# Kernel tuning notes

Measured on AMD Instinct MI355X. Metric: run time of the kernel, lower is better.

## Reference

```python
import jax, jax.numpy as jnp
import numpy as np
import math

D_MODEL = 64
N_HEADS = 4
D_HEAD = D_MODEL // N_HEADS
SCALE = math.sqrt(D_HEAD)
B, NQ, NK = 32, 16384, 31


def setup_inputs() -> dict:
    key = jax.random.key(0)
    kq, kk, kv, km, kw, kb = jax.random.split(key, 6)
    Q = jax.random.normal(kq, (B, NQ, D_MODEL), dtype=jnp.float32)
    K = jax.random.normal(kk, (B, NK, D_MODEL), dtype=jnp.float32)
    V = jax.random.normal(kv, (B, NK, D_MODEL), dtype=jnp.float32)
    mask = jax.random.randint(km, (B, NK), 0, 2).astype(jnp.bool_)
    # out_proj: nn.Linear(d_model, d_model)
    lim = 1.0 / math.sqrt(D_MODEL)
    W_out = jax.random.uniform(kw, (D_MODEL, D_MODEL), minval=-lim, maxval=lim, dtype=jnp.float32)
    b_out = jax.random.uniform(kb, (D_MODEL,), minval=-lim, maxval=lim, dtype=jnp.float32)
    return {"Q": Q, "K": K, "V": V, "mask": mask, "W_out": W_out, "b_out": b_out}


def reference(Q, K, V, mask, W_out, b_out):
    Bn, Nq, D = Q.shape
    Nk = K.shape[1]
    # (B, H, N, d_head)
    q = Q.reshape(Bn, Nq, N_HEADS, D_HEAD).transpose(0, 2, 1, 3)
    k = K.reshape(Bn, Nk, N_HEADS, D_HEAD).transpose(0, 2, 1, 3)
    v = V.reshape(Bn, Nk, N_HEADS, D_HEAD).transpose(0, 2, 1, 3)
    # (B, H, Nq, Nk)
    attn = jnp.einsum('bhqd,bhkd->bhqk', q, k) / SCALE
    attn = jnp.where(mask[:, None, None, :], attn, -jnp.inf)
    attn = jax.nn.softmax(attn, axis=-1)
    attn = jnp.nan_to_num(attn, nan=0.0)
    out = jnp.einsum('bhqk,bhkd->bhqd', attn, v)
    out = out.transpose(0, 2, 1, 3).reshape(Bn, Nq, D)
    return out @ W_out.T + b_out
```

## Files before the change

kernel.cpp:

```cpp
#include <hip/hip_runtime.h>
#include <math.h>

typedef _Float16 half4_t __attribute__((ext_vector_type(4)));
typedef __fp16   fp16x2  __attribute__((ext_vector_type(2)));
typedef float    f32x4   __attribute__((ext_vector_type(4)));

#define B_   32
#define NQ_  16384
#define NK_  31
#define DM_  64

static __device__ __forceinline__ half4_t cvt4(f32x4 f) {
  fp16x2 lo = __builtin_amdgcn_cvt_pkrtz(f[0], f[1]);
  fp16x2 hi = __builtin_amdgcn_cvt_pkrtz(f[2], f[3]);
  half4_t r;
  r[0] = (_Float16)lo[0]; r[1] = (_Float16)lo[1];
  r[2] = (_Float16)hi[0]; r[3] = (_Float16)hi[1];
  return r;
}

__global__ __launch_bounds__(256) void attn(
    const float* __restrict__ Q, const float* __restrict__ K,
    const float* __restrict__ V, const unsigned char* __restrict__ mraw,
    const float* __restrict__ W, const float* __restrict__ bout,
    float* __restrict__ out) {
  int b    = blockIdx.x >> 5;
  int blk  = blockIdx.x & 31;
  int tid  = threadIdx.x;
  int wave = tid >> 6, lane = tid & 63;
  int lq = lane & 15, quad = lane >> 4;

  unsigned mb;
  {
    unsigned char c0 = 0, c1 = 0;
    if (lane < 62) { c0 = mraw[2 * lane]; c1 = mraw[2 * lane + 1]; }
    unsigned long long m3f =
        __ballot(lane < 62 && (c0 == 0x3f || c1 == 0x3f));
    unsigned long long moff =
        __ballot(lane < 62 && ((((2 * lane) & 3) != 0 && c0 != 0) || c1 != 0));
    int mode = m3f ? 2 : (moff ? 0 : 1);
    int nz = 0;
    if (lane < NK_) {
      int idx = b * NK_ + lane;
      nz = (mode == 0) ? (mraw[idx] != 0)
         : (mode == 1) ? (((const int*)mraw)[idx] != 0)
                       : (((const float*)mraw)[idx] != 0.0f);
    }
    mb = (unsigned)__ballot(nz) & 0x7fffffffu;
  }

  f32x4 cbias[2];
  #pragma unroll
  for (int tt = 0; tt < 2; ++tt)
    #pragma unroll
    for (int r = 0; r < 4; ++r) {
      int key = 16 * tt + 4 * quad + r;
      cbias[tt][r] = ((mb >> key) & 1u) ? 0.0f : -1e30f;
    }

  const f32x4 fzero = {0.f, 0.f, 0.f, 0.f};

  half4_t kf[2][4];
  #pragma unroll
  for (int tt = 0; tt < 2; ++tt) {
    int k = 16 * tt + lq;
    #pragma unroll
    for (int h = 0; h < 4; ++h) {
      f32x4 f = fzero;
      if (k < NK_)
        f = *(const f32x4*)(K + ((size_t)b * NK_ + k) * DM_ + 16 * h + 4 * quad);
      kf[tt][h] = cvt4(f * 0.25f);
    }
  }

  half4_t vwf[4][8];
  {
    half4_t af[8];
    #pragma unroll
    for (int s = 0; s < 8; ++s) {
      int k = 16 * (s & 1) + lq, h = s >> 1;
      f32x4 f = fzero;
      if (k < NK_)
        f = *(const f32x4*)(V + ((size_t)b * NK_ + k) * DM_ + 16 * h + 4 * quad);
      af[s] = cvt4(f);
    }
    half4_t bf[4][4];
    #pragma unroll
    for (int dt = 0; dt < 4; ++dt)
      #pragma unroll
      for (int h = 0; h < 4; ++h) {
        f32x4 f = *(const f32x4*)(W + (16 * dt + lq) * DM_ + 16 * h + 4 * quad);
        bf[dt][h] = cvt4(f);
      }
    #pragma unroll
    for (int dt = 0; dt < 4; ++dt)
      #pragma unroll
      for (int s = 0; s < 8; ++s) {
        f32x4 m = __builtin_amdgcn_mfma_f32_16x16x16f16(af[s], bf[dt][s >> 1],
                                                        fzero, 0, 0, 0);
        vwf[dt][s] = cvt4(m);
      }
  }

  f32x4 bias[4];
  #pragma unroll
  for (int dt = 0; dt < 4; ++dt)
    bias[dt] = *(const f32x4*)(bout + 16 * dt + 4 * quad);

  int w = blk * 4 + wave;
  const float* qrow = Q + ((size_t)b * NQ_ + lq) * DM_ + 4 * quad;

  f32x4 qraw[4];
  #pragma unroll
  for (int h = 0; h < 4; ++h)
    qraw[h] = *(const f32x4*)(qrow + (size_t)(w * 16) * DM_ + 16 * h);

  #pragma unroll 1
  for (int it = 0; it < 8; ++it) {
    int q0 = (w + it * 128) * 16;

    f32x4 qnext[4];
    if (it < 7) {
      #pragma unroll
      for (int h = 0; h < 4; ++h)
        qnext[h] = *(const f32x4*)(qrow + (size_t)(q0 + 2048) * DM_ + 16 * h);
    }

    half4_t qf[4];
    #pragma unroll
    for (int h = 0; h < 4; ++h) qf[h] = cvt4(qraw[h]);

    half4_t pf[8];
    #pragma unroll
    for (int h = 0; h < 4; ++h) {
      f32x4 c0 = __builtin_amdgcn_mfma_f32_16x16x16f16(kf[0][h], qf[h], cbias[0], 0, 0, 0);
      f32x4 c1 = __builtin_amdgcn_mfma_f32_16x16x16f16(kf[1][h], qf[h], cbias[1], 0, 0, 0);
      f32x4 e0, e1;
      #pragma unroll
      for (int r = 0; r < 4; ++r) { e0[r] = __expf(c0[r]); e1[r] = __expf(c1[r]); }
      float sum = (e0[0] + e0[1]) + (e0[2] + e0[3]) +
                  (e1[0] + e1[1]) + (e1[2] + e1[3]);
      sum += __shfl_xor(sum, 16);
      sum += __shfl_xor(sum, 32);
      float inv = (sum > 0.f) ? __builtin_amdgcn_rcpf(sum) : 0.f;
      pf[2 * h + 0] = cvt4(e0 * inv);
      pf[2 * h + 1] = cvt4(e1 * inv);
    }

    f32x4 acc[4] = {fzero, fzero, fzero, fzero};
    #pragma unroll
    for (int s = 0; s < 8; ++s)
      #pragma unroll
      for (int dt = 0; dt < 4; ++dt)
        acc[dt] = __builtin_amdgcn_mfma_f32_16x16x16f16(vwf[dt][s], pf[s], acc[dt], 0, 0, 0);

    float* obase = out + ((size_t)b * NQ_ + q0 + lq) * DM_ + 4 * quad;
    #pragma unroll
    for (int dt = 0; dt < 4; ++dt)
      *(f32x4*)(obase + 16 * dt) = acc[dt] + bias[dt];

    if (it < 7) {
      #pragma unroll
      for (int h = 0; h < 4; ++h) qraw[h] = qnext[h];
    }
  }
}

extern "C" void kernel_launch(void* const* d_in, const int* in_sizes, int n_in,
                              void* d_out, int out_size, void* d_ws, size_t ws_size,
                              hipStream_t stream) {
  const float*         Q    = (const float*)d_in[0];
  const float*         K    = (const float*)d_in[1];
  const float*         V    = (const float*)d_in[2];
  const unsigned char* mask = (const unsigned char*)d_in[3];
  const float*         W    = (const float*)d_in[4];
  const float*         bo   = (const float*)d_in[5];
  float*               out  = (float*)d_out;

  hipLaunchKernelGGL(attn, dim3(B_ * 32), dim3(256), 0, stream,
                     Q, K, V, mask, W, bo, out);
}
```

Measured before the change: 255.8 us.

## Share K and V·W fragments across waves via LDS and double the grid

```diff
diff --git a/kernel.cpp b/kernel.cpp
--- a/kernel.cpp
+++ b/kernel.cpp
@@ -2,6 +2,7 @@
 #include <math.h>
 
 typedef _Float16 half4_t __attribute__((ext_vector_type(4)));
+typedef _Float16 half8_t __attribute__((ext_vector_type(8)));
 typedef __fp16   fp16x2  __attribute__((ext_vector_type(2)));
 typedef float    f32x4   __attribute__((ext_vector_type(4)));
 
@@ -9,6 +10,8 @@
 #define NQ_  16384
 #define NK_  31
 #define DM_  64
+#define BLK_PER_B 64
+#define ITERS 4
 
 static __device__ __forceinline__ half4_t cvt4(f32x4 f) {
   fp16x2 lo = __builtin_amdgcn_cvt_pkrtz(f[0], f[1]);
@@ -24,11 +27,16 @@
     const float* __restrict__ V, const unsigned char* __restrict__ mraw,
     const float* __restrict__ W, const float* __restrict__ bout,
     float* __restrict__ out) {
-  int b    = blockIdx.x >> 5;
-  int blk  = blockIdx.x & 31;
+  int b    = blockIdx.x >> 6;
+  int blk  = blockIdx.x & 63;
   int tid  = threadIdx.x;
   int wave = tid >> 6, lane = tid & 63;
   int lq = lane & 15, quad = lane >> 4;
+
+  __shared__ half8_t lds_kf[4][64];
+  __shared__ half8_t lds_vw[8][2][64];
+
+  const f32x4 fzero = {0.f, 0.f, 0.f, 0.f};
 
   unsigned mb;
   {
@@ -58,22 +66,17 @@
       cbias[tt][r] = ((mb >> key) & 1u) ? 0.0f : -1e30f;
     }
 
-  const f32x4 fzero = {0.f, 0.f, 0.f, 0.f};
-
-  half4_t kf[2][4];
   #pragma unroll
-  for (int tt = 0; tt < 2; ++tt) {
-    int k = 16 * tt + lq;
-    #pragma unroll
-    for (int h = 0; h < 4; ++h) {
-      f32x4 f = fzero;
-      if (k < NK_)
-        f = *(const f32x4*)(K + ((size_t)b * NK_ + k) * DM_ + 16 * h + 4 * quad);
-      kf[tt][h] = cvt4(f * 0.25f);
-    }
+  for (int j = 0; j < 2; ++j) {
+    int f  = wave * 2 + j;
+    int tt = f >> 2, h = f & 3;
+    int k  = 16 * tt + lq;
+    f32x4 fv = fzero;
+    if (k < NK_)
+      fv = *(const f32x4*)(K + ((size_t)b * NK_ + k) * DM_ + 16 * h + 4 * quad);
+    ((half4_t*)&lds_kf[h][lane])[tt] = cvt4(fv * 0.25f);
   }
 
-  half4_t vwf[4][8];
   {
     half4_t af[8];
     #pragma unroll
@@ -84,28 +87,26 @@
         f = *(const f32x4*)(V + ((size_t)b * NK_ + k) * DM_ + 16 * h + 4 * quad);
       af[s] = cvt4(f);
     }
-    half4_t bf[4][4];
+    half4_t bf[4];
     #pragma unroll
-    for (int dt = 0; dt < 4; ++dt)
-      #pragma unroll
-      for (int h = 0; h < 4; ++h) {
-        f32x4 f = *(const f32x4*)(W + (16 * dt + lq) * DM_ + 16 * h + 4 * quad);
-        bf[dt][h] = cvt4(f);
-      }
+    for (int h = 0; h < 4; ++h) {
+      f32x4 f = *(const f32x4*)(W + (16 * wave + lq) * DM_ + 16 * h + 4 * quad);
+      bf[h] = cvt4(f);
+    }
     #pragma unroll
-    for (int dt = 0; dt < 4; ++dt)
-      #pragma unroll
-      for (int s = 0; s < 8; ++s) {
-        f32x4 m = __builtin_amdgcn_mfma_f32_16x16x16f16(af[s], bf[dt][s >> 1],
-                                                        fzero, 0, 0, 0);
-        vwf[dt][s] = cvt4(m);
-      }
+    for (int s = 0; s < 8; ++s) {
+      f32x4 m = __builtin_amdgcn_mfma_f32_16x16x16f16(af[s], bf[s >> 1],
+                                                      fzero, 0, 0, 0);
+      ((half4_t*)&lds_vw[s][wave >> 1][lane])[wave & 1] = cvt4(m);
+    }
   }
 
   f32x4 bias[4];
   #pragma unroll
   for (int dt = 0; dt < 4; ++dt)
     bias[dt] = *(const f32x4*)(bout + 16 * dt + 4 * quad);
+
+  __syncthreads();
 
   int w = blk * 4 + wave;
   const float* qrow = Q + ((size_t)b * NQ_ + lq) * DM_ + 4 * quad;
@@ -116,14 +117,14 @@
     qraw[h] = *(const f32x4*)(qrow + (size_t)(w * 16) * DM_ + 16 * h);
 
   #pragma unroll 1
-  for (int it = 0; it < 8; ++it) {
-    int q0 = (w + it * 128) * 16;
+  for (int it = 0; it < ITERS; ++it) {
+    int q0 = (w + it * 256) * 16;
 
     f32x4 qnext[4];
-    if (it < 7) {
+    if (it < ITERS - 1) {
       #pragma unroll
       for (int h = 0; h < 4; ++h)
-        qnext[h] = *(const f32x4*)(qrow + (size_t)(q0 + 2048) * DM_ + 16 * h);
+        qnext[h] = *(const f32x4*)(qrow + (size_t)(q0 + 4096) * DM_ + 16 * h);
     }
 
     half4_t qf[4];
@@ -133,8 +134,11 @@
     half4_t pf[8];
     #pragma unroll
     for (int h = 0; h < 4; ++h) {
-      f32x4 c0 = __builtin_amdgcn_mfma_f32_16x16x16f16(kf[0][h], qf[h], cbias[0], 0, 0, 0);
-      f32x4 c1 = __builtin_amdgcn_mfma_f32_16x16x16f16(kf[1][h], qf[h], cbias[1], 0, 0, 0);
+      half8_t kk = lds_kf[h][lane];
+      half4_t k0 = __builtin_shufflevector(kk, kk, 0, 1, 2, 3);
+      half4_t k1 = __builtin_shufflevector(kk, kk, 4, 5, 6, 7);
+      f32x4 c0 = __builtin_amdgcn_mfma_f32_16x16x16f16(k0, qf[h], cbias[0], 0, 0, 0);
+      f32x4 c1 = __builtin_amdgcn_mfma_f32_16x16x16f16(k1, qf[h], cbias[1], 0, 0, 0);
       f32x4 e0, e1;
       #pragma unroll
       for (int r = 0; r < 4; ++r) { e0[r] = __expf(c0[r]); e1[r] = __expf(c1[r]); }
@@ -149,17 +153,25 @@
 
     f32x4 acc[4] = {fzero, fzero, fzero, fzero};
     #pragma unroll
-    for (int s = 0; s < 8; ++s)
-      #pragma unroll
-      for (int dt = 0; dt < 4; ++dt)
-        acc[dt] = __builtin_amdgcn_mfma_f32_16x16x16f16(vwf[dt][s], pf[s], acc[dt], 0, 0, 0);
+    for (int s = 0; s < 8; ++s) {
+      half8_t v01 = lds_vw[s][0][lane];
+      half8_t v23 = lds_vw[s][1][lane];
+      half4_t a0 = __builtin_shufflevector(v01, v01, 0, 1, 2, 3);
+      half4_t a1 = __builtin_shufflevector(v01, v01, 4, 5, 6, 7);
+      half4_t a2 = __builtin_shufflevector(v23, v23, 0, 1, 2, 3);
+      half4_t a3 = __builtin_shufflevector(v23, v23, 4, 5, 6, 7);
+      acc[0] = __builtin_amdgcn_mfma_f32_16x16x16f16(a0, pf[s], acc[0], 0, 0, 0);
+      acc[1] = __builtin_amdgcn_mfma_f32_16x16x16f16(a1, pf[s], acc[1], 0, 0, 0);
+      acc[2] = __builtin_amdgcn_mfma_f32_16x16x16f16(a2, pf[s], acc[2], 0, 0, 0);
+      acc[3] = __builtin_amdgcn_mfma_f32_16x16x16f16(a3, pf[s], acc[3], 0, 0, 0);
+    }
 
     float* obase = out + ((size_t)b * NQ_ + q0 + lq) * DM_ + 4 * quad;
     #pragma unroll
     for (int dt = 0; dt < 4; ++dt)
       *(f32x4*)(obase + 16 * dt) = acc[dt] + bias[dt];
 
-    if (it < 7) {
+    if (it < ITERS - 1) {
       #pragma unroll
       for (int h = 0; h < 4; ++h) qraw[h] = qnext[h];
     }
@@ -177,6 +189,6 @@
   const float*         bo   = (const float*)d_in[5];
   float*               out  = (float*)d_out;
 
-  hipLaunchKernelGGL(attn, dim3(B_ * 32), dim3(256), 0, stream,
+  hipLaunchKernelGGL(attn, dim3(B_ * BLK_PER_B), dim3(256), 0, stream,
                      Q, K, V, mask, W, bo, out);
 }
```

Result: faster. 248.9 us (-2.7%).

## Share V·W product via LDS, process two query tiles per iteration, use exp2

Applied to the files above, without the earlier changes.

```diff
diff --git a/kernel.cpp b/kernel.cpp
--- a/kernel.cpp
+++ b/kernel.cpp
@@ -2,6 +2,7 @@
 #include <math.h>
 
 typedef _Float16 half4_t __attribute__((ext_vector_type(4)));
+typedef _Float16 half8_t __attribute__((ext_vector_type(8)));
 typedef __fp16   fp16x2  __attribute__((ext_vector_type(2)));
 typedef float    f32x4   __attribute__((ext_vector_type(4)));
 
@@ -9,6 +10,9 @@
 #define NQ_  16384
 #define NK_  31
 #define DM_  64
+#define BLK_PER_B 32
+#define PAIRS 4
+#define KSCALE 0.3606738222635048f
 
 static __device__ __forceinline__ half4_t cvt4(f32x4 f) {
   fp16x2 lo = __builtin_amdgcn_cvt_pkrtz(f[0], f[1]);
@@ -19,7 +23,7 @@
   return r;
 }
 
-__global__ __launch_bounds__(256) void attn(
+__global__ __launch_bounds__(256, 3) void attn(
     const float* __restrict__ Q, const float* __restrict__ K,
     const float* __restrict__ V, const unsigned char* __restrict__ mraw,
     const float* __restrict__ W, const float* __restrict__ bout,
@@ -29,6 +33,20 @@
   int tid  = threadIdx.x;
   int wave = tid >> 6, lane = tid & 63;
   int lq = lane & 15, quad = lane >> 4;
+
+  __shared__ half8_t lds_vw[8][2][64];
+
+  const f32x4 fzero = {0.f, 0.f, 0.f, 0.f};
+
+  int w = blk * 4 + wave;
+  const float* qrow = Q + ((size_t)b * NQ_ + lq) * DM_ + 4 * quad;
+
+  f32x4 qA[4], qB[4];
+  #pragma unroll
+  for (int h = 0; h < 4; ++h) {
+    qA[h] = *(const f32x4*)(qrow + (size_t)(w * 16) * DM_ + 16 * h);
+    qB[h] = *(const f32x4*)(qrow + (size_t)((w + 128) * 16) * DM_ + 16 * h);
+  }
 
   unsigned mb;
   {
@@ -58,8 +76,6 @@
       cbias[tt][r] = ((mb >> key) & 1u) ? 0.0f : -1e30f;
     }
 
-  const f32x4 fzero = {0.f, 0.f, 0.f, 0.f};
-
   half4_t kf[2][4];
   #pragma unroll
   for (int tt = 0; tt < 2; ++tt) {
@@ -69,11 +85,10 @@
       f32x4 f = fzero;
       if (k < NK_)
         f = *(const f32x4*)(K + ((size_t)b * NK_ + k) * DM_ + 16 * h + 4 * quad);
-      kf[tt][h] = cvt4(f * 0.25f);
-    }
-  }
-
-  half4_t vwf[4][8];
+      kf[tt][h] = cvt4(f * KSCALE);
+    }
+  }
+
   {
     half4_t af[8];
     #pragma unroll
@@ -84,22 +99,18 @@
         f = *(const f32x4*)(V + ((size_t)b * NK_ + k) * DM_ + 16 * h + 4 * quad);
       af[s] = cvt4(f);
     }
-    half4_t bf[4][4];
-    #pragma unroll
-    for (int dt = 0; dt < 4; ++dt)
-      #pragma unroll
-      for (int h = 0; h < 4; ++h) {
-        f32x4 f = *(const f32x4*)(W + (16 * dt + lq) * DM_ + 16 * h + 4 * quad);
-        bf[dt][h] = cvt4(f);
-      }
-    #pragma unroll
-    for (int dt = 0; dt < 4; ++dt)
-      #pragma unroll
-      for (int s = 0; s < 8; ++s) {
-        f32x4 m = __builtin_amdgcn_mfma_f32_16x16x16f16(af[s], bf[dt][s >> 1],
-                                                        fzero, 0, 0, 0);
-        vwf[dt][s] = cvt4(m);
-      }
+    half4_t bf[4];
+    #pragma unroll
+    for (int h = 0; h < 4; ++h) {
+      f32x4 f = *(const f32x4*)(W + (16 * wave + lq) * DM_ + 16 * h + 4 * quad);
+      bf[h] = cvt4(f);
+    }
+    #pragma unroll
+    for (int s = 0; s < 8; ++s) {
+      f32x4 m = __builtin_amdgcn_mfma_f32_16x16x16f16(af[s], bf[s >> 1],
+                                                      fzero, 0, 0, 0);
+      ((half4_t*)&lds_vw[s][wave >> 1][lane])[wave & 1] = cvt4(m);
+    }
   }
 
   f32x4 bias[4];
@@ -107,61 +118,100 @@
   for (int dt = 0; dt < 4; ++dt)
     bias[dt] = *(const f32x4*)(bout + 16 * dt + 4 * quad);
 
-  int w = blk * 4 + wave;
-  const float* qrow = Q + ((size_t)b * NQ_ + lq) * DM_ + 4 * quad;
-
-  f32x4 qraw[4];
-  #pragma unroll
-  for (int h = 0; h < 4; ++h)
-    qraw[h] = *(const f32x4*)(qrow + (size_t)(w * 16) * DM_ + 16 * h);
-
-  #pragma unroll 1
-  for (int it = 0; it < 8; ++it) {
-    int q0 = (w + it * 128) * 16;
-
-    f32x4 qnext[4];
-    if (it < 7) {
-      #pragma unroll
-      for (int h = 0; h < 4; ++h)
-        qnext[h] = *(const f32x4*)(qrow + (size_t)(q0 + 2048) * DM_ + 16 * h);
-    }
-
-    half4_t qf[4];
-    #pragma unroll
-    for (int h = 0; h < 4; ++h) qf[h] = cvt4(qraw[h]);
-
-    half4_t pf[8];
+  __syncthreads();
+
+  #pragma unroll
+  for (int p = 0; p < PAIRS; ++p) {
+    half4_t qfA[4], qfB[4];
+    #pragma unroll
+    for (int h = 0; h < 4; ++h) { qfA[h] = cvt4(qA[h]); qfB[h] = cvt4(qB[h]); }
+
+    f32x4 qnA[4], qnB[4];
+    if (p + 1 < PAIRS) {
+      #pragma unroll
+      for (int h = 0; h < 4; ++h) {
+        qnA[h] = *(const f32x4*)(
+            qrow + (size_t)((w + (2 * p + 2) * 128) * 16) * DM_ + 16 * h);
+        qnB[h] = *(const f32x4*)(
+            qrow + (size_t)((w + (2 * p + 3) * 128) * 16) * DM_ + 16 * h);
+      }
+    }
+
+    f32x4 accA[4] = {bias[0], bias[1], bias[2], bias[3]};
+    f32x4 accB[4] = {bias[0], bias[1], bias[2], bias[3]};
+
     #pragma unroll
     for (int h = 0; h < 4; ++h) {
-      f32x4 c0 = __builtin_amdgcn_mfma_f32_16x16x16f16(kf[0][h], qf[h], cbias[0], 0, 0, 0);
-      f32x4 c1 = __builtin_amdgcn_mfma_f32_16x16x16f16(kf[1][h], qf[h], cbias[1], 0, 0, 0);
-      f32x4 e0, e1;
-      #pragma unroll
-      for (int r = 0; r < 4; ++r) { e0[r] = __expf(c0[r]); e1[r] = __expf(c1[r]); }
-      float sum = (e0[0] + e0[1]) + (e0[2] + e0[3]) +
-                  (e1[0] + e1[1]) + (e1[2] + e1[3]);
-      sum += __shfl_xor(sum, 16);
-      sum += __shfl_xor(sum, 32);
-      float inv = (sum > 0.f) ? __builtin_amdgcn_rcpf(sum) : 0.f;
-      pf[2 * h + 0] = cvt4(e0 * inv);
-      pf[2 * h + 1] = cvt4(e1 * inv);
-    }
-
-    f32x4 acc[4] = {fzero, fzero, fzero, fzero};
-    #pragma unroll
-    for (int s = 0; s < 8; ++s)
-      #pragma unroll
-      for (int dt = 0; dt < 4; ++dt)
-        acc[dt] = __builtin_amdgcn_mfma_f32_16x16x16f16(vwf[dt][s], pf[s], acc[dt], 0, 0, 0);
-
-    float* obase = out + ((size_t)b * NQ_ + q0 + lq) * DM_ + 4 * quad;
-    #pragma unroll
-    for (int dt = 0; dt < 4; ++dt)
-      *(f32x4*)(obase + 16 * dt) = acc[dt] + bias[dt];
-
-    if (it < 7) {
-      #pragma unroll
-      for (int h = 0; h < 4; ++h) qraw[h] = qnext[h];
+      f32x4 c0A = __builtin_amdgcn_mfma_f32_16x16x16f16(kf[0][h], qfA[h], cbias[0], 0, 0, 0);
+      f32x4 c1A = __builtin_amdgcn_mfma_f32_16x16x16f16(kf[1][h], qfA[h], cbias[1], 0, 0, 0);
+      f32x4 c0B = __builtin_amdgcn_mfma_f32_16x16x16f16(kf[0][h], qfB[h], cbias[0], 0, 0, 0);
+      f32x4 c1B = __builtin_amdgcn_mfma_f32_16x16x16f16(kf[1][h], qfB[h], cbias[1], 0, 0, 0);
+
+      f32x4 e0A, e1A, e0B, e1B;
+      #pragma unroll
+      for (int r = 0; r < 4; ++r) {
+        e0A[r] = __builtin_amdgcn_exp2f(c0A[r]);
+        e1A[r] = __builtin_amdgcn_exp2f(c1A[r]);
+        e0B[r] = __builtin_amdgcn_exp2f(c0B[r]);
+        e1B[r] = __builtin_amdgcn_exp2f(c1B[r]);
+      }
+      float sA = (e0A[0] + e0A[1]) + (e0A[2] + e0A[3]) +
+                 (e1A[0] + e1A[1]) + (e1A[2] + e1A[3]);
+      float sB = (e0B[0] + e0B[1]) + (e0B[2] + e0B[3]) +
+                 (e1B[0] + e1B[1]) + (e1B[2] + e1B[3]);
+      sA += __shfl_xor(sA, 16);  sB += __shfl_xor(sB, 16);
+      sA += __shfl_xor(sA, 32);  sB += __shfl_xor(sB, 32);
+      float iA = (sA > 0.f) ? __builtin_amdgcn_rcpf(sA) : 0.f;
+      float iB = (sB > 0.f) ? __builtin_amdgcn_rcpf(sB) : 0.f;
+      half4_t pA0 = cvt4(e0A * iA), pA1 = cvt4(e1A * iA);
+      half4_t pB0 = cvt4(e0B * iB), pB1 = cvt4(e1B * iB);
+
+      half8_t u0 = lds_vw[2 * h + 0][0][lane];
+      half8_t u1 = lds_vw[2 * h + 0][1][lane];
+      half8_t v0 = lds_vw[2 * h + 1][0][lane];
+      half8_t v1 = lds_vw[2 * h + 1][1][lane];
+      half4_t s0d0 = __builtin_shufflevector(u0, u0, 0, 1, 2, 3);
+      half4_t s0d1 = __builtin_shufflevector(u0, u0, 4, 5, 6, 7);
+      half4_t s0d2 = __builtin_shufflevector(u1, u1, 0, 1, 2, 3);
+      half4_t s0d3 = __builtin_shufflevector(u1, u1, 4, 5, 6, 7);
+      half4_t s1d0 = __builtin_shufflevector(v0, v0, 0, 1, 2, 3);
+      half4_t s1d1 = __builtin_shufflevector(v0, v0, 4, 5, 6, 7);
+      half4_t s1d2 = __builtin_shufflevector(v1, v1, 0, 1, 2, 3);
+      half4_t s1d3 = __builtin_shufflevector(v1, v1, 4, 5, 6, 7);
+
+      accA[0] = __builtin_amdgcn_mfma_f32_16x16x16f16(s0d0, pA0, accA[0], 0, 0, 0);
+      accA[1] = __builtin_amdgcn_mfma_f32_16x16x16f16(s0d1, pA0, accA[1], 0, 0, 0);
+      accA[2] = __builtin_amdgcn_mfma_f32_16x16x16f16(s0d2, pA0, accA[2], 0, 0, 0);
+      accA[3] = __builtin_amdgcn_mfma_f32_16x16x16f16(s0d3, pA0, accA[3], 0, 0, 0);
+      accB[0] = __builtin_amdgcn_mfma_f32_16x16x16f16(s0d0, pB0, accB[0], 0, 0, 0);
+      accB[1] = __builtin_amdgcn_mfma_f32_16x16x16f16(s0d1, pB0, accB[1], 0, 0, 0);
+      accB[2] = __builtin_amdgcn_mfma_f32_16x16x16f16(s0d2, pB0, accB[2], 0, 0, 0);
+      accB[3] = __builtin_amdgcn_mfma_f32_16x16x16f16(s0d3, pB0, accB[3], 0, 0, 0);
+      accA[0] = __builtin_amdgcn_mfma_f32_16x16x16f16(s1d0, pA1, accA[0], 0, 0, 0);
+      accA[1] = __builtin_amdgcn_mfma_f32_16x16x16f16(s1d1, pA1, accA[1], 0, 0, 0);
+      accA[2] = __builtin_amdgcn_mfma_f32_16x16x16f16(s1d2, pA1, accA[2], 0, 0, 0);
+      accA[3] = __builtin_amdgcn_mfma_f32_16x16x16f16(s1d3, pA1, accA[3], 0, 0, 0);
+      accB[0] = __builtin_amdgcn_mfma_f32_16x16x16f16(s1d0, pB1, accB[0], 0, 0, 0);
+      accB[1] = __builtin_amdgcn_mfma_f32_16x16x16f16(s1d1, pB1, accB[1], 0, 0, 0);
+      accB[2] = __builtin_amdgcn_mfma_f32_16x16x16f16(s1d2, pB1, accB[2], 0, 0, 0);
+      accB[3] = __builtin_amdgcn_mfma_f32_16x16x16f16(s1d3, pB1, accB[3], 0, 0, 0);
+    }
+
+    {
+      int q0A = (w + (2 * p + 0) * 128) * 16;
+      int q0B = (w + (2 * p + 1) * 128) * 16;
+      float* oA = out + ((size_t)b * NQ_ + q0A + lq) * DM_ + 4 * quad;
+      float* oB = out + ((size_t)b * NQ_ + q0B + lq) * DM_ + 4 * quad;
+      #pragma unroll
+      for (int dt = 0; dt < 4; ++dt) {
+        *(f32x4*)(oA + 16 * dt) = accA[dt];
+        *(f32x4*)(oB + 16 * dt) = accB[dt];
+      }
+    }
+
+    if (p + 1 < PAIRS) {
+      #pragma unroll
+      for (int h = 0; h < 4; ++h) { qA[h] = qnA[h]; qB[h] = qnB[h]; }
     }
   }
 }
@@ -177,6 +227,6 @@
   const float*         bo   = (const float*)d_in[5];
   float*               out  = (float*)d_out;
 
-  hipLaunchKernelGGL(attn, dim3(B_ * 32), dim3(256), 0, stream,
+  hipLaunchKernelGGL(attn, dim3(B_ * BLK_PER_B), dim3(256), 0, stream,
                      Q, K, V, mask, W, bo, out);
 }
```

Measured after the change: 250.7 us. 2.0% less time.
